# Kernel tuning notes

Measured on AMD Instinct MI355X. Metric: run time of the kernel, lower is better.

## Reference

```python
import jax, jax.numpy as jnp
import numpy as np
from jax import lax

B, A, K = 16, 200000, 300          # batch, anchors, NMS candidate cap
THR_CONF, THR_NMS = 0.5, 0.3
VAR0, VAR1 = 0.1, 0.2              # RetinaFace decode variances


def setup_inputs() -> dict:
    key = jax.random.key(0)
    k1, k2, k3, k4, k5 = jax.random.split(key, 5)
    p_loc = jax.random.normal(k1, (B, A, 4), jnp.float32) * 0.5
    p_conf = jax.random.normal(k2, (B, A, 1), jnp.float32) - 2.0
    p_landms = jax.random.normal(k3, (B, A, 10), jnp.float32) * 0.5
    cxy = jax.random.uniform(k4, (A, 2), jnp.float32)
    wh = 0.01 + 0.09 * jax.random.uniform(k5, (A, 2), jnp.float32)
    anchors = jnp.concatenate([cxy, wh], axis=-1)   # [A,4] cx,cy,w,h in [0,1]
    return {"p_loc": p_loc, "p_conf": p_conf, "p_landms": p_landms, "anchors": anchors}


def _decode_boxes_ltrb(anchors, loc):
    # fix_bbox: cxy = a_cxy + loc[:2]*0.1*a_wh ; wh = a_wh * exp(loc[2:]*0.2)
    a = anchors[None]                              # [1,A,4]
    cxy = a[..., :2] + loc[..., :2] * VAR0 * a[..., 2:]
    wh = a[..., 2:] * jnp.exp(loc[..., 2:] * VAR1)
    half = 0.5 * wh
    return jnp.concatenate([cxy - half, cxy + half], axis=-1)  # xywh2ltrb -> [B,A,4]


def _decode_keypoints(anchors, landms):
    # fix_keypoints: 5 points, each a_cxy + d*0.1*a_wh (computed in original fwd; unused in outputs)
    a = anchors[None]
    d = landms.reshape(landms.shape[0], landms.shape[1], 5, 2)
    kp = a[..., None, :2] + d * VAR0 * a[..., None, 2:]
    return kp.reshape(landms.shape)


def _iou_matrix(b):  # b [K,4] ltrb -> [K,K]
    lt = jnp.maximum(b[:, None, :2], b[None, :, :2])
    rb = jnp.minimum(b[:, None, 2:], b[None, :, 2:])
    wh = jnp.clip(rb - lt, 0.0)
    inter = wh[..., 0] * wh[..., 1]
    area = jnp.clip(b[:, 2] - b[:, 0], 0.0) * jnp.clip(b[:, 3] - b[:, 1], 0.0)
    union = area[:, None] + area[None, :] - inter
    return inter / jnp.maximum(union, 1e-9)


def _nms_keep(boxes, valid):
    # boxes already sorted by descending score; greedy NMS over K candidates
    iou = _iou_matrix(boxes)
    idx = jnp.arange(K)
    def body(i, keep):
        sup = keep[i] & (iou[i] > THR_NMS) & (idx > i)
        return keep & ~sup
    return lax.fori_loop(0, K, body, valid)


def reference(p_loc, p_conf, p_landms, anchors):
    scores = jax.nn.sigmoid(p_conf[..., 0])                     # [B,A]
    boxes_ltrb = _decode_boxes_ltrb(anchors, p_loc)             # [B,A,4]
    _ = _decode_keypoints(anchors, p_landms)                    # faithful dead compute

    mask = scores >= THR_CONF
    masked_scores = jnp.where(mask, scores, 0.0)
    top_scores, top_idx = lax.top_k(masked_scores, K)           # [B,K] sorted desc
    top_boxes = jnp.take_along_axis(boxes_ltrb, top_idx[..., None], axis=1)  # [B,K,4]
    valid = top_scores >= THR_CONF

    keep = jax.vmap(_nms_keep)(top_boxes, valid)                # [B,K] bool
    keep_f = keep.astype(top_scores.dtype)

    ids_batch2 = jnp.where(keep, jnp.broadcast_to(jnp.arange(B)[:, None], (B, K)), -1).reshape(-1)
    p_boxes_ltrb2 = (top_boxes * keep_f[..., None]).reshape(-1, 4)
    p_scores2 = (top_scores * keep_f).reshape(-1)
    p_labels2 = keep_f.reshape(-1)   # original labels are all ones; zero on padded slots
    return ids_batch2, p_boxes_ltrb2, p_labels2, p_scores2, keep.reshape(-1)
```

## Files before the change

### kernel.cpp

```cpp
#include <hip/hip_runtime.h>
#include <cstdint>

typedef unsigned int u32;
typedef unsigned long long u64;

#define B 16
#define A 200000
#define K 300
#define CAP 8192

__global__ __launch_bounds__(256) void scan_kernel(const float* __restrict__ p_conf,
                                                   u64* __restrict__ cand,
                                                   u32* __restrict__ cnt) {
    __shared__ u64 lbuf[1024];
    __shared__ u32 lcnt;
    __shared__ u32 lbase;
    const int b = blockIdx.y;
    const int f4 = blockIdx.x * 256 + threadIdx.x;

    if (threadIdx.x == 0) lcnt = 0;
    __syncthreads();

    if (f4 < A / 4) {
        const float4 c4 = ((const float4*)(p_conf + (size_t)b * A))[f4];
        const float xs[4] = {c4.x, c4.y, c4.z, c4.w};
        #pragma unroll
        for (int e = 0; e < 4; ++e) {
            const float x = xs[e];
            if (x >= -0.001f) {
                float s = 1.0f / (1.0f + expf(-x));
                if (s >= 0.5f) {
                    u32 sb  = __float_as_uint(s);
                    u32 idx = (u32)(f4 * 4 + e);
                    u64 key = ((u64)sb << 32) | (u64)(0xFFFFFFFFu - idx);
                    u32 p = atomicAdd(&lcnt, 1u);
                    lbuf[p] = key;
                }
            }
        }
    }
    __syncthreads();
    if (threadIdx.x == 0 && lcnt > 0) lbase = atomicAdd(&cnt[b], lcnt);
    __syncthreads();
    const u32 total = lcnt;
    for (u32 t = threadIdx.x; t < total; t += 256) {
        u32 g = lbase + t;
        if (g < CAP) cand[(size_t)b * CAP + g] = lbuf[t];
    }
}

__global__ __launch_bounds__(512) void select_nms_kernel(
    const float* __restrict__ p_loc,
    const float* __restrict__ anchors,
    const u64* __restrict__ cand,
    const u32* __restrict__ cnt,
    float* __restrict__ out) {

    __shared__ u32 hist[512];
    __shared__ u32 sfx[512];
    __shared__ u32 wsum[8];
    __shared__ u64 buf[1024];
    __shared__ u64 skey[K];
    __shared__ float4 bx4[K];
    __shared__ float barea[K];
    __shared__ u64 mask[K][5];
    __shared__ u64 keepw[5];
    __shared__ u32 sh_cut, sh_m;

    const int b    = blockIdx.x;
    const int tid  = threadIdx.x;
    const int lane = tid & 63;
    const int wv   = tid >> 6;
    const u32 c    = min(cnt[b], (u32)CAP);
    const u32 need = min((u32)K, c);
    const u64* mycand = cand + (size_t)b * CAP;

    hist[tid] = 0;
    {   u64* mf = &mask[0][0];
        for (int i = tid; i < K * 5; i += 512) mf[i] = 0ull; }
    if (tid == 0) { sh_m = 0; sh_cut = 0; }
    __syncthreads();

    for (u32 i = tid; i < c; i += 512) {
        u32 sb  = (u32)(mycand[i] >> 32);
        u32 bin = min((sb - 0x3F000000u) >> 14, 511u);
        atomicAdd(&hist[bin], 1u);
    }
    __syncthreads();

    u32 s = hist[tid];
    #pragma unroll
    for (int off = 1; off < 64; off <<= 1) {
        u32 t = __shfl_down(s, off, 64);
        if (lane + off < 64) s += t;
    }
    if (lane == 0) wsum[wv] = s;
    __syncthreads();
    u32 tail = 0;
    #pragma unroll
    for (int w = 0; w < 8; ++w) if (w > wv) tail += wsum[w];
    sfx[tid] = s + tail;
    __syncthreads();

    if (need > 0) {
        if (sfx[tid] >= need && (tid == 511 || sfx[tid + 1] < need)) sh_cut = (u32)tid;
    }
    __syncthreads();

    const u32 cut = sh_cut;
    for (u32 i = tid; i < c; i += 512) {
        u64 kk  = mycand[i];
        u32 sb  = (u32)(kk >> 32);
        u32 bin = min((sb - 0x3F000000u) >> 14, 511u);
        if (bin >= cut) {
            u32 p = atomicAdd(&sh_m, 1u);
            if (p < 1024) buf[p] = kk;
        }
    }
    __syncthreads();
    const u32 M = min(sh_m, 1024u);

    for (u32 t = tid; t < M; t += 512) {
        const u64 mykey = buf[t];
        u32 r = 0;
        #pragma unroll 4
        for (u32 j = 0; j < M; ++j) r += (buf[j] > mykey) ? 1u : 0u;
        if (r < (u32)K) skey[r] = mykey;
    }
    __syncthreads();

    const u32 S = need;
    float dl = 0.f, dt = 0.f, dr = 0.f, db = 0.f, dsc = 0.f;
    if (tid < K) {
        float ar = 0.f;
        if ((u32)tid < S) {
            u64 kk = skey[tid];
            dsc = __uint_as_float((u32)(kk >> 32));
            u32 aidx = 0xFFFFFFFFu - (u32)(kk & 0xFFFFFFFFull);
            const float4 loc = ((const float4*)p_loc)[(size_t)b * A + aidx];
            const float4 an  = ((const float4*)anchors)[aidx];
            float cx = an.x + loc.x * 0.1f * an.z;
            float cy = an.y + loc.y * 0.1f * an.w;
            float w  = an.z * expf(loc.z * 0.2f);
            float h  = an.w * expf(loc.w * 0.2f);
            dl = cx - 0.5f * w; dt = cy - 0.5f * h;
            dr = cx + 0.5f * w; db = cy + 0.5f * h;
            ar = fmaxf(dr - dl, 0.0f) * fmaxf(db - dt, 0.0f);
        }
        bx4[tid] = make_float4(dl, dt, dr, db);
        barea[tid] = ar;
    }
    __syncthreads();

    {
        int r, j0, st; bool active;
        if (tid < K) { r = tid;     j0 = r + 1; st = (r < 212) ? 2 : 1; active = ((u32)r < S); }
        else         { r = tid - K; j0 = r + 2; st = 2;                 active = ((u32)r < S); }
        if (active) {
            const float4 bi = bx4[r];
            const float  ai = barea[r];
            u64 acc = 0; int wcur = j0 >> 6;
            for (int j = j0; j < (int)S; j += st) {
                const int w = j >> 6;
                if (w != wcur) {
                    if (acc) atomicOr(&mask[r][wcur], acc);
                    acc = 0; wcur = w;
                }
                const float4 bj = bx4[j];
                float lt0 = fmaxf(bi.x, bj.x);
                float lt1 = fmaxf(bi.y, bj.y);
                float rb0 = fminf(bi.z, bj.z);
                float rb1 = fminf(bi.w, bj.w);
                float iw = fmaxf(rb0 - lt0, 0.0f);
                float ih = fmaxf(rb1 - lt1, 0.0f);
                float inter = iw * ih;
                float uni = ai + barea[j] - inter;
                float iou = inter / fmaxf(uni, 1e-9f);
                if (iou > 0.3f) acc |= (1ull << (j & 63));
            }
            if (acc) atomicOr(&mask[r][wcur], acc);
        }
    }
    __syncthreads();

    if (tid == 0) {
        u64 k0, k1, k2, k3, k4;
        {
            int rem;
            rem = (int)S - 0;   k0 = rem <= 0 ? 0ull : (rem >= 64 ? ~0ull : ((1ull << rem) - 1ull));
            rem = (int)S - 64;  k1 = rem <= 0 ? 0ull : (rem >= 64 ? ~0ull : ((1ull << rem) - 1ull));
            rem = (int)S - 128; k2 = rem <= 0 ? 0ull : (rem >= 64 ? ~0ull : ((1ull << rem) - 1ull));
            rem = (int)S - 192; k3 = rem <= 0 ? 0ull : (rem >= 64 ? ~0ull : ((1ull << rem) - 1ull));
            rem = (int)S - 256; k4 = rem <= 0 ? 0ull : (rem >= 64 ? ~0ull : ((1ull << rem) - 1ull));
        }
        auto nms_chunk = [&](u64& kw, int wi) {
            int lim = (int)S - wi * 64; if (lim > 64) lim = 64;
            #pragma unroll 8
            for (int bq = 0; bq < lim; ++bq) {
                const u64* row = mask[wi * 64 + bq];
                u64 c0 = row[0], c1 = row[1], c2 = row[2], c3 = row[3], c4v = row[4];
                u64 sl = ((kw >> bq) & 1ull) ? ~0ull : 0ull;
                k0 &= ~(c0 & sl); k1 &= ~(c1 & sl); k2 &= ~(c2 & sl);
                k3 &= ~(c3 & sl); k4 &= ~(c4v & sl);
            }
        };
        nms_chunk(k0, 0); nms_chunk(k1, 1); nms_chunk(k2, 2);
        nms_chunk(k3, 3); nms_chunk(k4, 4);
        keepw[0] = k0; keepw[1] = k1; keepw[2] = k2; keepw[3] = k3; keepw[4] = k4;
    }
    __syncthreads();

    if (tid < K) {
        const int g = b * K + tid;
        const bool kept = (keepw[tid >> 6] >> (tid & 63)) & 1ull;
        out[g] = kept ? (float)b : -1.0f;
        float* obox = out + B * K + (size_t)g * 4;
        obox[0] = kept ? dl : 0.0f;
        obox[1] = kept ? dt : 0.0f;
        obox[2] = kept ? dr : 0.0f;
        obox[3] = kept ? db : 0.0f;
        out[B * K * 5 + g] = kept ? 1.0f : 0.0f;
        out[B * K * 6 + g] = kept ? dsc : 0.0f;
        out[B * K * 7 + g] = kept ? 1.0f : 0.0f;
    }
}

extern "C" void kernel_launch(void* const* d_in, const int* in_sizes, int n_in,
                              void* d_out, int out_size, void* d_ws, size_t ws_size,
                              hipStream_t stream) {
    const float* p_loc   = (const float*)d_in[0];
    const float* p_conf  = (const float*)d_in[1];
    const float* anchors = (const float*)d_in[3];
    float* out = (float*)d_out;

    u64* cand = (u64*)d_ws;
    u32* cnt  = (u32*)((char*)d_ws + (size_t)B * CAP * 8);

    hipMemsetAsync(cnt, 0, B * sizeof(u32), stream);

    dim3 gridA((A / 4 + 255) / 256, B);
    scan_kernel<<<gridA, 256, 0, stream>>>(p_conf, cand, cnt);
    select_nms_kernel<<<B, 512, 0, stream>>>(p_loc, anchors, cand, cnt, out);
}
```

Baseline: 285.4 us.

## Defer sigmoid to select kernel, cache candidates in registers, use SoA boxes

Measured after the change: 474.0 us. +66.1%, slower.

```diff
diff --git a/kernel.cpp b/kernel.cpp
--- a/kernel.cpp
+++ b/kernel.cpp
@@ -28,14 +28,11 @@
         for (int e = 0; e < 4; ++e) {
             const float x = xs[e];
             if (x >= -0.001f) {
-                float s = 1.0f / (1.0f + expf(-x));
-                if (s >= 0.5f) {
-                    u32 sb  = __float_as_uint(s);
-                    u32 idx = (u32)(f4 * 4 + e);
-                    u64 key = ((u64)sb << 32) | (u64)(0xFFFFFFFFu - idx);
-                    u32 p = atomicAdd(&lcnt, 1u);
-                    lbuf[p] = key;
-                }
+                u32 xb  = __float_as_uint(x);
+                u32 idx = (u32)(f4 * 4 + e);
+                u64 key = ((u64)xb << 32) | (u64)(0xFFFFFFFFu - idx);
+                u32 p = atomicAdd(&lcnt, 1u);
+                lbuf[p] = key;
             }
         }
     }
@@ -61,8 +58,7 @@
     __shared__ u32 wsum[8];
     __shared__ u64 buf[1024];
     __shared__ u64 skey[K];
-    __shared__ float4 bx4[K];
-    __shared__ float barea[K];
+    __shared__ float sl[K], st_[K], sr[K], sb_[K], sar[K];
     __shared__ u64 mask[K][5];
     __shared__ u64 keepw[5];
     __shared__ u32 sh_cut, sh_m;
@@ -72,7 +68,6 @@
     const int lane = tid & 63;
     const int wv   = tid >> 6;
     const u32 c    = min(cnt[b], (u32)CAP);
-    const u32 need = min((u32)K, c);
     const u64* mycand = cand + (size_t)b * CAP;
 
     hist[tid] = 0;
@@ -81,10 +76,22 @@
     if (tid == 0) { sh_m = 0; sh_cut = 0; }
     __syncthreads();
 
-    for (u32 i = tid; i < c; i += 512) {
-        u32 sb  = (u32)(mycand[i] >> 32);
-        u32 bin = min((sb - 0x3F000000u) >> 14, 511u);
-        atomicAdd(&hist[bin], 1u);
+    u64 kreg[16];
+    #pragma unroll
+    for (int q = 0; q < 16; ++q) {
+        kreg[q] = 0;
+        const u32 i = (u32)(q * 512 + tid);
+        if (i < c) {
+            const u64 kk = mycand[i];
+            const float x = __uint_as_float((u32)(kk >> 32));
+            const float s = 1.0f / (1.0f + expf(-x));
+            const u32 sb = __float_as_uint(s);
+            if (sb >= 0x3F000000u) {
+                const u32 bin = min((sb - 0x3F000000u) >> 14, 511u);
+                atomicAdd(&hist[bin], 1u);
+                kreg[q] = ((u64)sb << 32) | (kk & 0xFFFFFFFFull);
+            }
+        }
     }
     __syncthreads();
 
@@ -102,19 +109,22 @@
     sfx[tid] = s + tail;
     __syncthreads();
 
+    const u32 need = min((u32)K, sfx[0]);
     if (need > 0) {
         if (sfx[tid] >= need && (tid == 511 || sfx[tid + 1] < need)) sh_cut = (u32)tid;
     }
     __syncthreads();
 
     const u32 cut = sh_cut;
-    for (u32 i = tid; i < c; i += 512) {
-        u64 kk  = mycand[i];
-        u32 sb  = (u32)(kk >> 32);
-        u32 bin = min((sb - 0x3F000000u) >> 14, 511u);
-        if (bin >= cut) {
-            u32 p = atomicAdd(&sh_m, 1u);
-            if (p < 1024) buf[p] = kk;
+    #pragma unroll
+    for (int q = 0; q < 16; ++q) {
+        const u64 kk = kreg[q];
+        if (kk != 0ull) {
+            const u32 bin = min(((u32)(kk >> 32) - 0x3F000000u) >> 14, 511u);
+            if (bin >= cut) {
+                u32 p = atomicAdd(&sh_m, 1u);
+                if (p < 1024) buf[p] = kk;
+            }
         }
     }
     __syncthreads();
@@ -147,34 +157,31 @@
             dr = cx + 0.5f * w; db = cy + 0.5f * h;
             ar = fmaxf(dr - dl, 0.0f) * fmaxf(db - dt, 0.0f);
         }
-        bx4[tid] = make_float4(dl, dt, dr, db);
-        barea[tid] = ar;
+        sl[tid] = dl; st_[tid] = dt; sr[tid] = dr; sb_[tid] = db; sar[tid] = ar;
     }
     __syncthreads();
 
     {
-        int r, j0, st; bool active;
-        if (tid < K) { r = tid;     j0 = r + 1; st = (r < 212) ? 2 : 1; active = ((u32)r < S); }
-        else         { r = tid - K; j0 = r + 2; st = 2;                 active = ((u32)r < S); }
+        int r, j0, jstep; bool active;
+        if (tid < K) { r = tid;     j0 = r + 1; jstep = (r < 212) ? 2 : 1; active = ((u32)r < S); }
+        else         { r = tid - K; j0 = r + 2; jstep = 2;                 active = ((u32)r < S); }
         if (active) {
-            const float4 bi = bx4[r];
-            const float  ai = barea[r];
+            const float li = sl[r], ti = st_[r], ri = sr[r], bi = sb_[r], ai = sar[r];
             u64 acc = 0; int wcur = j0 >> 6;
-            for (int j = j0; j < (int)S; j += st) {
+            for (int j = j0; j < (int)S; j += jstep) {
                 const int w = j >> 6;
                 if (w != wcur) {
                     if (acc) atomicOr(&mask[r][wcur], acc);
                     acc = 0; wcur = w;
                 }
-                const float4 bj = bx4[j];
-                float lt0 = fmaxf(bi.x, bj.x);
-                float lt1 = fmaxf(bi.y, bj.y);
-                float rb0 = fminf(bi.z, bj.z);
-                float rb1 = fminf(bi.w, bj.w);
+                float lt0 = fmaxf(li, sl[j]);
+                float lt1 = fmaxf(ti, st_[j]);
+                float rb0 = fminf(ri, sr[j]);
+                float rb1 = fminf(bi, sb_[j]);
                 float iw = fmaxf(rb0 - lt0, 0.0f);
                 float ih = fmaxf(rb1 - lt1, 0.0f);
                 float inter = iw * ih;
-                float uni = ai + barea[j] - inter;
+                float uni = ai + sar[j] - inter;
                 float iou = inter / fmaxf(uni, 1e-9f);
                 if (iou > 0.3f) acc |= (1ull << (j & 63));
             }
@@ -199,9 +206,9 @@
             for (int bq = 0; bq < lim; ++bq) {
                 const u64* row = mask[wi * 64 + bq];
                 u64 c0 = row[0], c1 = row[1], c2 = row[2], c3 = row[3], c4v = row[4];
-                u64 sl = ((kw >> bq) & 1ull) ? ~0ull : 0ull;
-                k0 &= ~(c0 & sl); k1 &= ~(c1 & sl); k2 &= ~(c2 & sl);
-                k3 &= ~(c3 & sl); k4 &= ~(c4v & sl);
+                u64 slm = ((kw >> bq) & 1ull) ? ~0ull : 0ull;
+                k0 &= ~(c0 & slm); k1 &= ~(c1 & slm); k2 &= ~(c2 & slm);
+                k3 &= ~(c3 & slm); k4 &= ~(c4v & slm);
             }
         };
         nms_chunk(k0, 0); nms_chunk(k1, 1); nms_chunk(k2, 2);
```
